# Kernel tuning notes

Hardware: AMD Instinct MI355X
Metric: run time of the kernel (lower is better)

The kernel has to match this reference:

```python
import jax, jax.numpy as jnp
import numpy as np

DIM = 768      # input_size
H = 8          # num_heads
HD = 8         # hidden_size (per-head assoc dim)
SCALING = 0.25 # beta
STEPS = 5      # update_steps_max
B = 65536


def setup_inputs() -> dict:
    key = jax.random.key(0)
    ks = jax.random.split(key, 6)
    s = 0.02
    return {
        "x": jax.random.normal(ks[0], (B, DIM), jnp.float32),
        "q_state": jax.random.normal(ks[1], (1, 1, DIM), jnp.float32) * s,
        "Wq": jax.random.normal(ks[2], (H * HD, DIM), jnp.float32) * s,
        "bq": jnp.zeros((H * HD,), jnp.float32),
        "Wk": jax.random.normal(ks[3], (H * HD, DIM), jnp.float32) * s,
        "bk": jnp.zeros((H * HD,), jnp.float32),
        "Wv": jax.random.normal(ks[4], (H * HD, DIM), jnp.float32) * s,
        "bv": jnp.zeros((H * HD,), jnp.float32),
        "Wo": jax.random.normal(ks[5], (DIM, H * HD), jnp.float32) * s,
        "bo": jnp.zeros((DIM,), jnp.float32),
    }


def reference(x, q_state, Wq, bq, Wk, bk, Wv, bv, Wo, bo):
    # x: (B, dim) -> stored patterns Y: (B, S=1, dim)
    Bn = x.shape[0]
    y = x[:, None, :]
    # projections: (B, S, H*HD) -> (B, H, S, HD)
    k = (y @ Wk.T + bk).reshape(Bn, 1, H, HD).transpose(0, 2, 1, 3)
    v = (y @ Wv.T + bv).reshape(Bn, 1, H, HD).transpose(0, 2, 1, 3)
    # learnable state pattern (quantity=1) projected to query, broadcast over batch
    q = (q_state @ Wq.T + bq).reshape(1, 1, H, HD)           # (1, 1, H, HD)
    q = jnp.broadcast_to(q, (Bn, 1, H, HD)).transpose(0, 2, 1, 3)  # (B, H, 1, HD)

    def assoc(qq):  # beta-scaled Hopfield association matrix (B, H, 1, S)
        return jax.nn.softmax(SCALING * jnp.einsum('bhqd,bhsd->bhqs', qq, k), axis=-1)

    # iterative Hopfield state refinement: xi = softmax(beta * (xi K) K^T)
    xi0 = assoc(q)

    def step(xi, _):
        qq = jnp.einsum('bhqs,bhsd->bhqd', xi, k)
        return assoc(qq), None

    xi, _ = jax.lax.scan(step, xi0, None, length=STEPS)
    out = jnp.einsum('bhqs,bhsd->bhqd', xi, v)               # (B, H, 1, HD)
    out = out.transpose(0, 2, 1, 3).reshape(Bn, H * HD)      # (B, H*HD)
    return out @ Wo.T + bo                                   # (B, dim)
```

## Files before the change

kernel.cpp:

```cpp
#include <hip/hip_runtime.h>


#define DIM 768
#define NB  64
#define KC  (DIM / 32)
#define RPW 32
#define WPB 2
#define RPB (RPW * WPB)
#define WV_ELEMS (NB * DIM)

typedef __attribute__((ext_vector_type(8))) short short8;
typedef __attribute__((ext_vector_type(4))) float f32x4;

__device__ __forceinline__ unsigned short f2bf(float f) {
    union { float f; unsigned int u; } v; v.f = f;
    return (unsigned short)((v.u + 0x7fffu + ((v.u >> 16) & 1u)) >> 16);
}

__device__ __forceinline__ short8 pack_bf8(float4 lo, float4 hi) {
    short8 r;
    r[0] = (short)f2bf(lo.x); r[1] = (short)f2bf(lo.y);
    r[2] = (short)f2bf(lo.z); r[3] = (short)f2bf(lo.w);
    r[4] = (short)f2bf(hi.x); r[5] = (short)f2bf(hi.y);
    r[6] = (short)f2bf(hi.z); r[7] = (short)f2bf(hi.w);
    return r;
}

__global__ void pack_weights(const float* __restrict__ Wv, const float* __restrict__ Wo,
                             unsigned short* __restrict__ pWv, unsigned short* __restrict__ pWo) {
    int e = blockIdx.x * 256 + threadIdx.x;
    int which = (e >= WV_ELEMS) ? 1 : 0;
    int idx = which ? e - WV_ELEMS : e;
    int frag = idx >> 9;
    int lane = (idx >> 3) & 63;
    int j = idx & 7;
    int lm = lane & 15, lq = lane >> 4;
    float v;
    if (!which) {
        int kc = frag >> 2, t = frag & 3;
        v = Wv[(t * 16 + lm) * DIM + kc * 32 + lq * 8 + j];
    } else {
        int tile = frag >> 1, h = frag & 1;
        v = Wo[(tile * 16 + lm) * NB + h * 32 + lq * 8 + j];
    }
    (which ? pWo : pWv)[idx] = f2bf(v);
}

__global__ __launch_bounds__(128, 4)
void pr_main(const float* __restrict__ x,
             const unsigned short* __restrict__ pWv, const float* __restrict__ bv,
             const unsigned short* __restrict__ pWo, const float* __restrict__ bo,
             float* __restrict__ out)
{
    __shared__ unsigned short sV[WPB][RPW][72];

    const int tid  = threadIdx.x;
    const int wave = tid >> 6;
    const int lane = tid & 63;
    const int lq   = lane >> 4;
    const int lm   = lane & 15;
    const long row0 = (long)blockIdx.x * RPB + wave * RPW;

    f32x4 accV[2][4];
    #pragma unroll
    for (int s = 0; s < 2; ++s)
        #pragma unroll
        for (int t = 0; t < 4; ++t) accV[s][t] = (f32x4){0.f, 0.f, 0.f, 0.f};

    const float* xb0 = x + (row0 + lm) * DIM + lq * 8;
    const float* xb1 = xb0 + 16 * DIM;
    const short8* wv = (const short8*)pWv + lane;

    #pragma unroll 2
    for (int kc = 0; kc < KC; ++kc) {
        const float4 a0l = *(const float4*)(xb0 + kc * 32);
        const float4 a0h = *(const float4*)(xb0 + kc * 32 + 4);
        const float4 a1l = *(const float4*)(xb1 + kc * 32);
        const float4 a1h = *(const float4*)(xb1 + kc * 32 + 4);
        const short8 a0 = pack_bf8(a0l, a0h);
        const short8 a1 = pack_bf8(a1l, a1h);
        #pragma unroll
        for (int t = 0; t < 4; ++t) {
            const short8 b = wv[(kc * 4 + t) * 64];
            accV[0][t] = __builtin_amdgcn_mfma_f32_16x16x32_bf16(a0, b, accV[0][t], 0, 0, 0);
            accV[1][t] = __builtin_amdgcn_mfma_f32_16x16x32_bf16(a1, b, accV[1][t], 0, 0, 0);
        }
    }

    #pragma unroll
    for (int t = 0; t < 4; ++t) {
        const float bvn = bv[t * 16 + lm];
        #pragma unroll
        for (int s = 0; s < 2; ++s) {
            #pragma unroll
            for (int r = 0; r < 4; ++r) {
                sV[wave][s * 16 + lq * 4 + r][t * 16 + lm] = f2bf(accV[s][t][r] + bvn);
            }
        }
    }
    __syncthreads();
    short8 aV[2][2];
    #pragma unroll
    for (int s = 0; s < 2; ++s) {
        aV[s][0] = *(const short8*)&sV[wave][s * 16 + lm][lq * 8];
        aV[s][1] = *(const short8*)&sV[wave][s * 16 + lm][32 + lq * 8];
    }

    const short8* wo = (const short8*)pWo + lane;
    for (int cc = 0; cc < 12; ++cc) {
        f32x4 acc[2][4];
        #pragma unroll
        for (int s = 0; s < 2; ++s)
            #pragma unroll
            for (int t = 0; t < 4; ++t) acc[s][t] = (f32x4){0.f, 0.f, 0.f, 0.f};

        #pragma unroll
        for (int t = 0; t < 4; ++t) {
            const int tile = cc * 4 + t;
            const short8 b0 = wo[(tile * 2 + 0) * 64];
            const short8 b1 = wo[(tile * 2 + 1) * 64];
            #pragma unroll
            for (int s = 0; s < 2; ++s) {
                acc[s][t] = __builtin_amdgcn_mfma_f32_16x16x32_bf16(aV[s][0], b0, acc[s][t], 0, 0, 0);
                acc[s][t] = __builtin_amdgcn_mfma_f32_16x16x32_bf16(aV[s][1], b1, acc[s][t], 0, 0, 0);
            }
        }

        #pragma unroll
        for (int t = 0; t < 4; ++t) {
            const int col = cc * 64 + t * 16 + lm;
            const float boc = bo[col];
            #pragma unroll
            for (int s = 0; s < 2; ++s) {
                #pragma unroll
                for (int r = 0; r < 4; ++r) {
                    out[(row0 + s * 16 + lq * 4 + r) * DIM + col] = acc[s][t][r] + boc;
                }
            }
        }
    }
}

extern "C" void kernel_launch(void* const* d_in, const int* in_sizes, int n_in,
                              void* d_out, int out_size, void* d_ws, size_t ws_size,
                              hipStream_t stream) {
    const float* x  = (const float*)d_in[0];
    const float* Wv = (const float*)d_in[6];
    const float* bv = (const float*)d_in[7];
    const float* Wo = (const float*)d_in[8];
    const float* bo = (const float*)d_in[9];
    float* out = (float*)d_out;

    unsigned short* pWv = (unsigned short*)d_ws;
    unsigned short* pWo = pWv + WV_ELEMS;

    pack_weights<<<dim3(2 * WV_ELEMS / 256), dim3(256), 0, stream>>>(Wv, Wo, pWv, pWo);

    const int Bn = in_sizes[0] / DIM;
    pr_main<<<dim3(Bn / RPB), dim3(128), 0, stream>>>(x, pWv, bv, pWo, bo, out);
}
```

Before: 372.4 us.

## Software-pipeline x and weight loads, shrink rows per wave, add nontemporal I/O

Each wave now handles 16 rows instead of 32, with 4 waves per block. The K loop prefetches x four chunks ahead and Wv fragments two chunks ahead, and the output GEMM prefetches Wo fragments two column chunks ahead. Loads of x and stores of out use nontemporal hints to avoid polluting cache with streamed data. The block-wide barrier is removed because each wave only reads its own shared-memory slice. The costs are higher register pressure from the prefetch buffers and each loaded weight fragment being reused across half as many rows.

```diff
diff --git a/kernel.cpp b/kernel.cpp
--- a/kernel.cpp
+++ b/kernel.cpp
@@ -4,8 +4,8 @@
 #define DIM 768
 #define NB  64
 #define KC  (DIM / 32)
-#define RPW 32
-#define WPB 2
+#define RPW 16
+#define WPB 4
 #define RPB (RPW * WPB)
 #define WV_ELEMS (NB * DIM)
 
@@ -17,13 +17,17 @@
     return (unsigned short)((v.u + 0x7fffu + ((v.u >> 16) & 1u)) >> 16);
 }
 
-__device__ __forceinline__ short8 pack_bf8(float4 lo, float4 hi) {
+__device__ __forceinline__ short8 pack_bf8(f32x4 lo, f32x4 hi) {
     short8 r;
-    r[0] = (short)f2bf(lo.x); r[1] = (short)f2bf(lo.y);
-    r[2] = (short)f2bf(lo.z); r[3] = (short)f2bf(lo.w);
-    r[4] = (short)f2bf(hi.x); r[5] = (short)f2bf(hi.y);
-    r[6] = (short)f2bf(hi.z); r[7] = (short)f2bf(hi.w);
+    r[0] = (short)f2bf(lo[0]); r[1] = (short)f2bf(lo[1]);
+    r[2] = (short)f2bf(lo[2]); r[3] = (short)f2bf(lo[3]);
+    r[4] = (short)f2bf(hi[0]); r[5] = (short)f2bf(hi[1]);
+    r[6] = (short)f2bf(hi[2]); r[7] = (short)f2bf(hi[3]);
     return r;
+}
+
+__device__ __forceinline__ f32x4 ld_nt_f4(const float* p) {
+    return __builtin_nontemporal_load((const f32x4*)p);
 }
 
 __global__ void pack_weights(const float* __restrict__ Wv, const float* __restrict__ Wo,
@@ -46,7 +50,7 @@
     (which ? pWo : pWv)[idx] = f2bf(v);
 }
 
-__global__ __launch_bounds__(128, 4)
+__global__ __launch_bounds__(256, 4)
 void pr_main(const float* __restrict__ x,
              const unsigned short* __restrict__ pWv, const float* __restrict__ bv,
              const unsigned short* __restrict__ pWo, const float* __restrict__ bo,
@@ -61,69 +65,91 @@
     const int lm   = lane & 15;
     const long row0 = (long)blockIdx.x * RPB + wave * RPW;
 
-    f32x4 accV[2][4];
+    f32x4 accV[4];
     #pragma unroll
-    for (int s = 0; s < 2; ++s)
-        #pragma unroll
-        for (int t = 0; t < 4; ++t) accV[s][t] = (f32x4){0.f, 0.f, 0.f, 0.f};
+    for (int t = 0; t < 4; ++t) accV[t] = (f32x4){0.f, 0.f, 0.f, 0.f};
 
-    const float* xb0 = x + (row0 + lm) * DIM + lq * 8;
-    const float* xb1 = xb0 + 16 * DIM;
+    const float* xp = x + (row0 + lm) * DIM + lq * 8;
     const short8* wv = (const short8*)pWv + lane;
 
-    #pragma unroll 2
+    f32x4 aP[4][2];
+    short8 bP[2][4];
+    #pragma unroll
+    for (int i = 0; i < 4; ++i) {
+        aP[i][0] = ld_nt_f4(xp + i * 32);
+        aP[i][1] = ld_nt_f4(xp + i * 32 + 4);
+    }
+    #pragma unroll
+    for (int i = 0; i < 2; ++i)
+        #pragma unroll
+        for (int t = 0; t < 4; ++t) bP[i][t] = wv[(i * 4 + t) * 64];
+
+    #pragma unroll
     for (int kc = 0; kc < KC; ++kc) {
-        const float4 a0l = *(const float4*)(xb0 + kc * 32);
-        const float4 a0h = *(const float4*)(xb0 + kc * 32 + 4);
-        const float4 a1l = *(const float4*)(xb1 + kc * 32);
-        const float4 a1h = *(const float4*)(xb1 + kc * 32 + 4);
-        const short8 a0 = pack_bf8(a0l, a0h);
-        const short8 a1 = pack_bf8(a1l, a1h);
-        #pragma unroll
-        for (int t = 0; t < 4; ++t) {
-            const short8 b = wv[(kc * 4 + t) * 64];
-            accV[0][t] = __builtin_amdgcn_mfma_f32_16x16x32_bf16(a0, b, accV[0][t], 0, 0, 0);
-            accV[1][t] = __builtin_amdgcn_mfma_f32_16x16x32_bf16(a1, b, accV[1][t], 0, 0, 0);
+        const int sA = kc & 3, sB = kc & 1;
+        const f32x4 a_lo = aP[sA][0];
+        const f32x4 a_hi = aP[sA][1];
+        short8 b0 = bP[sB][0], b1 = bP[sB][1], b2 = bP[sB][2], b3 = bP[sB][3];
+        if (kc + 4 < KC) {
+            aP[sA][0] = ld_nt_f4(xp + (kc + 4) * 32);
+            aP[sA][1] = ld_nt_f4(xp + (kc + 4) * 32 + 4);
         }
+        if (kc + 2 < KC) {
+            #pragma unroll
+            for (int t = 0; t < 4; ++t) bP[sB][t] = wv[((kc + 2) * 4 + t) * 64];
+        }
+        const short8 a = pack_bf8(a_lo, a_hi);
+        accV[0] = __builtin_amdgcn_mfma_f32_16x16x32_bf16(a, b0, accV[0], 0, 0, 0);
+        accV[1] = __builtin_amdgcn_mfma_f32_16x16x32_bf16(a, b1, accV[1], 0, 0, 0);
+        accV[2] = __builtin_amdgcn_mfma_f32_16x16x32_bf16(a, b2, accV[2], 0, 0, 0);
+        accV[3] = __builtin_amdgcn_mfma_f32_16x16x32_bf16(a, b3, accV[3], 0, 0, 0);
     }
 
     #pragma unroll
     for (int t = 0; t < 4; ++t) {
         const float bvn = bv[t * 16 + lm];
         #pragma unroll
-        for (int s = 0; s < 2; ++s) {
+        for (int r = 0; r < 4; ++r) {
+            sV[wave][lq * 4 + r][t * 16 + lm] = f2bf(accV[t][r] + bvn);
+        }
+    }
+    short8 aV0 = *(const short8*)&sV[wave][lm][lq * 8];
+    short8 aV1 = *(const short8*)&sV[wave][lm][32 + lq * 8];
+
+    const short8* wo = (const short8*)pWo + lane;
+
+    short8 woP[2][8];
+    #pragma unroll
+    for (int i = 0; i < 2; ++i)
+        #pragma unroll
+        for (int t = 0; t < 4; ++t) {
+            woP[i][t * 2 + 0] = wo[((i * 4 + t) * 2 + 0) * 64];
+            woP[i][t * 2 + 1] = wo[((i * 4 + t) * 2 + 1) * 64];
+        }
+
+    #pragma unroll
+    for (int cc = 0; cc < 12; ++cc) {
+        const int s = cc & 1;
+        f32x4 acc[4];
+        #pragma unroll
+        for (int t = 0; t < 4; ++t) acc[t] = (f32x4){0.f, 0.f, 0.f, 0.f};
+
+        short8 cur[8];
+        #pragma unroll
+        for (int i = 0; i < 8; ++i) cur[i] = woP[s][i];
+
+        if (cc + 2 < 12) {
             #pragma unroll
-            for (int r = 0; r < 4; ++r) {
-                sV[wave][s * 16 + lq * 4 + r][t * 16 + lm] = f2bf(accV[s][t][r] + bvn);
+            for (int t = 0; t < 4; ++t) {
+                woP[s][t * 2 + 0] = wo[(((cc + 2) * 4 + t) * 2 + 0) * 64];
+                woP[s][t * 2 + 1] = wo[(((cc + 2) * 4 + t) * 2 + 1) * 64];
             }
         }
-    }
-    __syncthreads();
-    short8 aV[2][2];
-    #pragma unroll
-    for (int s = 0; s < 2; ++s) {
-        aV[s][0] = *(const short8*)&sV[wave][s * 16 + lm][lq * 8];
-        aV[s][1] = *(const short8*)&sV[wave][s * 16 + lm][32 + lq * 8];
-    }
-
-    const short8* wo = (const short8*)pWo + lane;
-    for (int cc = 0; cc < 12; ++cc) {
-        f32x4 acc[2][4];
-        #pragma unroll
-        for (int s = 0; s < 2; ++s)
-            #pragma unroll
-            for (int t = 0; t < 4; ++t) acc[s][t] = (f32x4){0.f, 0.f, 0.f, 0.f};
 
         #pragma unroll
         for (int t = 0; t < 4; ++t) {
-            const int tile = cc * 4 + t;
-            const short8 b0 = wo[(tile * 2 + 0) * 64];
-            const short8 b1 = wo[(tile * 2 + 1) * 64];
-            #pragma unroll
-            for (int s = 0; s < 2; ++s) {
-                acc[s][t] = __builtin_amdgcn_mfma_f32_16x16x32_bf16(aV[s][0], b0, acc[s][t], 0, 0, 0);
-                acc[s][t] = __builtin_amdgcn_mfma_f32_16x16x32_bf16(aV[s][1], b1, acc[s][t], 0, 0, 0);
-            }
+            acc[t] = __builtin_amdgcn_mfma_f32_16x16x32_bf16(aV0, cur[t * 2 + 0], acc[t], 0, 0, 0);
+            acc[t] = __builtin_amdgcn_mfma_f32_16x16x32_bf16(aV1, cur[t * 2 + 1], acc[t], 0, 0, 0);
         }
 
         #pragma unroll
@@ -131,11 +157,9 @@
             const int col = cc * 64 + t * 16 + lm;
             const float boc = bo[col];
             #pragma unroll
-            for (int s = 0; s < 2; ++s) {
-                #pragma unroll
-                for (int r = 0; r < 4; ++r) {
-                    out[(row0 + s * 16 + lq * 4 + r) * DIM + col] = acc[s][t][r] + boc;
-                }
+            for (int r = 0; r < 4; ++r) {
+                __builtin_nontemporal_store(acc[t][r] + boc,
+                    out + (row0 + lq * 4 + r) * DIM + col);
             }
         }
     }
@@ -157,5 +181,5 @@
     pack_weights<<<dim3(2 * WV_ELEMS / 256), dim3(256), 0, stream>>>(Wv, Wo, pWv, pWo);
 
     const int Bn = in_sizes[0] / DIM;
-    pr_main<<<dim3(Bn / RPB), dim3(128), 0, stream>>>(x, pWv, bv, pWo, bo, out);
+    pr_main<<<dim3(Bn / RPB), dim3(256), 0, stream>>>(x, pWv, bv, pWo, bo, out);
 }
```

Measured after the change: 412.7 us. +10.8%, slower.
